# Performance work log

Measured on AMD Instinct MI355X. Metric: run time of the kernel, lower is better.

## Reference

```python
import jax, jax.numpy as jnp
import numpy as np


def _haar_filters():
    s = 1.0 / np.sqrt(2.0).astype(np.float32)
    l = jnp.array([s, s], dtype=jnp.float32)
    h = jnp.array([-s, s], dtype=jnp.float32)
    ll = jnp.outer(l, l)
    lh = jnp.outer(h, l)
    hl = jnp.outer(l, h)
    hh = jnp.outer(h, h)
    # module registers ll, -lh, -hl, hh as buffers
    return ll, -lh, -hl, hh


def setup_inputs() -> dict:
    key = jax.random.key(0)
    x = jax.random.normal(key, (16, 12, 512, 512), dtype=jnp.float32)
    fll, flh, fhl, fhh = _haar_filters()
    return {"x": x, "fll": fll, "flh": flh, "fhl": fhl, "fhh": fhh}


def _upfirdn_band(x, f):
    # upfirdn2d(band, f, up_factor=2, padding=(1,0,1,0)):
    #   2) zero pad: 1 on left of W, 1 on top of H
    #   3) valid conv with 2x2 FIR filter, applied per channel
    #   4) down_factor=1 interpolate -> identity
    B, C, H, W = x.shape
    up = jax.image.resize(x, (B, C, 2 * H, 2 * W), method="bilinear")
    p = jnp.pad(up, ((0, 0), (0, 0), (1, 0), (1, 0)))  # [B,C,2H+1,2W+1]
    w = jnp.tile(f[None, None].astype(x.dtype), (C, 1, 1, 1))  # depthwise [C,1,2,2]
    return jax.lax.conv_general_dilated(
        p, w, window_strides=(1, 1), padding="VALID",
        feature_group_count=C,
        dimension_numbers=("NCHW", "OIHW", "NCHW"),
    )  # [B,C,2H,2W]


def reference(x, fll, flh, fhl, fhh):
    ll, lh, hl, hh = jnp.split(x, 4, axis=1)  # input.chunk(4, 1)
    out = (_upfirdn_band(ll, fll)
           + _upfirdn_band(lh, flh)
           + _upfirdn_band(hl, fhl)
           + _upfirdn_band(hh, fhh))
    return out
```

## Files before the change

kernel.cpp:

```cpp
#include <hip/hip_runtime.h>

namespace {

constexpr int Hh = 512, Ww = 512, OH = 1024, OW = 1024;
constexpr int NB_Y = 256;
constexpr int NBC  = 48;
constexpr int NWG  = NB_Y * NBC;

typedef float f32x4 __attribute__((ext_vector_type(4)));

__global__ __launch_bounds__(256) void ihaar(
    const float* __restrict__ x,
    const float* __restrict__ f0,
    const float* __restrict__ f1,
    const float* __restrict__ f2,
    const float* __restrict__ f3,
    float* __restrict__ out)
{
  const int bid = blockIdx.x;
  const int wg  = (bid & 7) * (NWG / 8) + (bid >> 3);
  const int bc   = wg / NB_Y;
  const int yblk = wg - bc * NB_Y;
  const int b = bc / 3;
  const int c = bc - 3 * b;

  const int t    = threadIdx.x;
  const int lane = t & 63;
  const int wv   = t >> 6;
  const int half = wv & 1;
  const int ty   = wv >> 1;
  const int y    = 2 * yblk + ty;
  const int x0   = half * 256 + lane * 4;

  const float4 F[4] = { *(const float4*)f0, *(const float4*)f1,
                        *(const float4*)f2, *(const float4*)f3 };

  const int u0r = (y > 0) ? y - 1 : 0;
  const int u2r = (y < Hh - 1) ? y + 1 : y;
  const bool needL = (lane == 0)  && (half == 1);
  const bool needR = (lane == 63) && (half == 0);
  const bool le = (x0 == 0), re = (x0 == Ww - 4);
  const int sc = needL ? (x0 - 1) : (x0 + 4);

  float Pe0=0.f,Pe1=0.f,Pe2=0.f,Pe3=0.f, Po0=0.f,Po1=0.f,Po2=0.f,Po3=0.f;
  float Qe0=0.f,Qe1=0.f,Qe2=0.f,Qe3=0.f, Qo0=0.f,Qo1=0.f,Qo2=0.f,Qo3=0.f;
  float SPe=0.f,SPo=0.f,SQe=0.f,SQo=0.f;

#define BAND(g, Ae0,Ae1,Ae2,Ae3, Ao0,Ao1,Ao2,Ao3, Se, So) { \
    const float uu0 = F[g].x, uu1 = F[g].z; \
    float pa0, pa1, pb0, pb1, pb2; \
    if (y > 0) { pa0 = 0.75f*uu0 + 0.25f*uu1; pa1 = 0.25f*uu0 + 0.75f*uu1; } \
    else       { pa0 = 0.f;                   pa1 = uu1; } \
    if (y == 0)           { pb0 = 0.f;         pb1 = uu0 + 0.75f*uu1; pb2 = 0.25f*uu1; } \
    else if (y == Hh - 1) { pb0 = 0.25f*uu0;   pb1 = 0.75f*uu0 + uu1; pb2 = 0.f; } \
    else                  { pb0 = 0.25f*uu0;   pb1 = 0.75f*(uu0+uu1); pb2 = 0.25f*uu1; } \
    const float* Xp = x + (size_t)(b * 12 + (g) * 3 + c) * (Hh * Ww); \
    const f32x4 q0 = *(const f32x4*)(Xp + (size_t)u0r * Ww + x0); \
    const f32x4 q1 = *(const f32x4*)(Xp + (size_t)y   * Ww + x0); \
    const f32x4 q2 = *(const f32x4*)(Xp + (size_t)u2r * Ww + x0); \
    Ae0 += pa0*q0.x + pa1*q1.x;  Ae1 += pa0*q0.y + pa1*q1.y; \
    Ae2 += pa0*q0.z + pa1*q1.z;  Ae3 += pa0*q0.w + pa1*q1.w; \
    Ao0 += pb0*q0.x + pb1*q1.x + pb2*q2.x; \
    Ao1 += pb0*q0.y + pb1*q1.y + pb2*q2.y; \
    Ao2 += pb0*q0.z + pb1*q1.z + pb2*q2.z; \
    Ao3 += pb0*q0.w + pb1*q1.w + pb2*q2.w; \
    if (needL || needR) { \
      const float s0 = Xp[(size_t)u0r * Ww + sc]; \
      const float s1 = Xp[(size_t)y   * Ww + sc]; \
      const float s2 = Xp[(size_t)u2r * Ww + sc]; \
      Se += pa0*s0 + pa1*s1;  So += pb0*s0 + pb1*s1 + pb2*s2; \
    } \
  }

  BAND(0, Pe0,Pe1,Pe2,Pe3, Po0,Po1,Po2,Po3, SPe, SPo)
  BAND(1, Pe0,Pe1,Pe2,Pe3, Po0,Po1,Po2,Po3, SPe, SPo)
  BAND(2, Qe0,Qe1,Qe2,Qe3, Qo0,Qo1,Qo2,Qo3, SQe, SQo)
  BAND(3, Qe0,Qe1,Qe2,Qe3, Qo0,Qo1,Qo2,Qo3, SQe, SQo)
#undef BAND

  float PeL = __shfl_up(Pe3, 1),  PoL = __shfl_up(Po3, 1);
  float QeL = __shfl_up(Qe3, 1),  QoL = __shfl_up(Qo3, 1);
  float PeR = __shfl_down(Pe0, 1), PoR = __shfl_down(Po0, 1);
  float QeR = __shfl_down(Qe0, 1), QoR = __shfl_down(Qo0, 1);
  if (needL) { PeL = SPe; PoL = SPo; QeL = SQe; QoL = SQo; }
  if (needR) { PeR = SPe; PoR = SPo; QeR = SQe; QoR = SQo; }

  const float vp = F[0].y * __builtin_amdgcn_rcpf(F[0].x);
  const float vq = F[2].y * __builtin_amdgcn_rcpf(F[2].x);
  const float h0p = 0.75f + 0.25f*vp, h1p = 0.25f + 0.75f*vp;
  const float g0p = 0.25f, g1p = 0.75f*(1.f + vp), g2p = 0.25f*vp;
  const float h0q = 0.75f + 0.25f*vq, h1q = 0.25f + 0.75f*vq;
  const float g0q = 0.25f, g1q = 0.75f*(1.f + vq), g2q = 0.25f*vq;
  const float h0pa = le ? 0.f : h0p, h1pa = le ? vp : h1p;
  const float g0pa = le ? 0.f : g0p, g1pa = le ? (1.f + 0.75f*vp) : g1p;
  const float g1pd = re ? (0.75f + vp) : g1p, g2pd = re ? 0.f : g2p;
  const float h0qa = le ? 0.f : h0q, h1qa = le ? vq : h1q;
  const float g0qa = le ? 0.f : g0q, g1qa = le ? (1.f + 0.75f*vq) : g1q;
  const float g1qd = re ? (0.75f + vq) : g1q, g2qd = re ? 0.f : g2q;

  const float e0 = h0pa*PeL + h1pa*Pe0           + h0qa*QeL + h1qa*Qe0;
  const float e1 = g0pa*PeL + g1pa*Pe0 + g2p*Pe1 + g0qa*QeL + g1qa*Qe0 + g2q*Qe1;
  const float e2 = h0p*Pe0  + h1p*Pe1            + h0q*Qe0  + h1q*Qe1;
  const float e3 = g0p*Pe0  + g1p*Pe1  + g2p*Pe2 + g0q*Qe0  + g1q*Qe1  + g2q*Qe2;
  const float e4 = h0p*Pe1  + h1p*Pe2            + h0q*Qe1  + h1q*Qe2;
  const float e5 = g0p*Pe1  + g1p*Pe2  + g2p*Pe3 + g0q*Qe1  + g1q*Qe2  + g2q*Qe3;
  const float e6 = h0p*Pe2  + h1p*Pe3            + h0q*Qe2  + h1q*Qe3;
  const float e7 = g0p*Pe2  + g1pd*Pe3 + g2pd*PeR+ g0q*Qe2  + g1qd*Qe3 + g2qd*QeR;
  const float o0 = h0pa*PoL + h1pa*Po0           + h0qa*QoL + h1qa*Qo0;
  const float o1 = g0pa*PoL + g1pa*Po0 + g2p*Po1 + g0qa*QoL + g1qa*Qo0 + g2q*Qo1;
  const float o2 = h0p*Po0  + h1p*Po1            + h0q*Qo0  + h1q*Qo1;
  const float o3 = g0p*Po0  + g1p*Po1  + g2p*Po2 + g0q*Qo0  + g1q*Qo1  + g2q*Qo2;
  const float o4 = h0p*Po1  + h1p*Po2            + h0q*Qo1  + h1q*Qo2;
  const float o5 = g0p*Po1  + g1p*Po2  + g2p*Po3 + g0q*Qo1  + g1q*Qo2  + g2q*Qo3;
  const float o6 = h0p*Po2  + h1p*Po3            + h0q*Qo2  + h1q*Qo3;
  const float o7 = g0p*Po2  + g1pd*Po3 + g2pd*PoR+ g0q*Qo2  + g1qd*Qo3 + g2qd*QoR;

  float* op = out + ((size_t)bc * OH + 2 * y) * OW + 2 * x0;
  const f32x4 E0 = { e0, e1, e2, e3 };
  const f32x4 E1 = { e4, e5, e6, e7 };
  const f32x4 O0 = { o0, o1, o2, o3 };
  const f32x4 O1 = { o4, o5, o6, o7 };
  __builtin_nontemporal_store(E0, (f32x4*)op);
  __builtin_nontemporal_store(E1, (f32x4*)(op + 4));
  __builtin_nontemporal_store(O0, (f32x4*)(op + OW));
  __builtin_nontemporal_store(O1, (f32x4*)(op + OW + 4));
}

}

extern "C" void kernel_launch(void* const* d_in, const int* in_sizes, int n_in,
                              void* d_out, int out_size, void* d_ws, size_t ws_size,
                              hipStream_t stream) {
  const float* x   = (const float*)d_in[0];
  const float* fll = (const float*)d_in[1];
  const float* flh = (const float*)d_in[2];
  const float* fhl = (const float*)d_in[3];
  const float* fhh = (const float*)d_in[4];
  float* out = (float*)d_out;

  ihaar<<<dim3(NWG), 256, 0, stream>>>(x, fll, flh, fhl, fhh, out);
}
```

Measured before the change: 68.11 us.

## Process two input rows per thread to share vertical halo loads

```diff
diff --git a/kernel.cpp b/kernel.cpp
--- a/kernel.cpp
+++ b/kernel.cpp
@@ -3,9 +3,9 @@
 namespace {
 
 constexpr int Hh = 512, Ww = 512, OH = 1024, OW = 1024;
-constexpr int NB_Y = 256;
-constexpr int NBC  = 48;
-constexpr int NWG  = NB_Y * NBC;
+constexpr int NB_YP = 128;
+constexpr int NBC   = 48;
+constexpr int NWG   = NB_YP * NBC;
 
 typedef float f32x4 __attribute__((ext_vector_type(4)));
 
@@ -19,8 +19,8 @@
 {
   const int bid = blockIdx.x;
   const int wg  = (bid & 7) * (NWG / 8) + (bid >> 3);
-  const int bc   = wg / NB_Y;
-  const int yblk = wg - bc * NB_Y;
+  const int bc  = wg / NB_YP;
+  const int ybp = wg - bc * NB_YP;
   const int b = bc / 3;
   const int c = bc - 3 * b;
 
@@ -28,62 +28,97 @@
   const int lane = t & 63;
   const int wv   = t >> 6;
   const int half = wv & 1;
-  const int ty   = wv >> 1;
-  const int y    = 2 * yblk + ty;
+  const int sub  = wv >> 1;
+  const int y0   = 4 * ybp + 2 * sub;
+  const int y1   = y0 + 1;
   const int x0   = half * 256 + lane * 4;
+
+  const int rm = (y0 > 0) ? y0 - 1 : 0;
+  const int rt = (y1 < Hh - 1) ? y1 + 1 : Hh - 1;
+
+  const bool needL = (lane == 0)  && (half == 1);
+  const bool needR = (lane == 63) && (half == 0);
+  const bool seam  = needL || needR;
+  const bool le = (x0 == 0), re = (x0 == Ww - 4);
+  const int sc = needL ? (x0 - 1) : (x0 + 4);
+
+  const size_t HW = (size_t)Hh * Ww;
+  const float* Xa = x + (size_t)(b * 12 + c) * HW;
+  const float* Xb = Xa + 3 * HW;
+  const float* Xc = Xa + 6 * HW;
+  const float* Xd = Xa + 9 * HW;
+  const size_t om = (size_t)rm * Ww + x0;
+  const size_t orr = (size_t)y0 * Ww + x0;
+  const size_t os = (size_t)y1 * Ww + x0;
+  const size_t ot = (size_t)rt * Ww + x0;
+
+  const f32x4 qAm = *(const f32x4*)(Xa + om), qAr = *(const f32x4*)(Xa + orr);
+  const f32x4 qAs = *(const f32x4*)(Xa + os), qAt = *(const f32x4*)(Xa + ot);
+  const f32x4 qBm = *(const f32x4*)(Xb + om), qBr = *(const f32x4*)(Xb + orr);
+  const f32x4 qBs = *(const f32x4*)(Xb + os), qBt = *(const f32x4*)(Xb + ot);
+  const f32x4 qCm = *(const f32x4*)(Xc + om), qCr = *(const f32x4*)(Xc + orr);
+  const f32x4 qCs = *(const f32x4*)(Xc + os), qCt = *(const f32x4*)(Xc + ot);
+  const f32x4 qDm = *(const f32x4*)(Xd + om), qDr = *(const f32x4*)(Xd + orr);
+  const f32x4 qDs = *(const f32x4*)(Xd + os), qDt = *(const f32x4*)(Xd + ot);
+
+  float sAm=0.f,sAr=0.f,sAs=0.f,sAt=0.f, sBm=0.f,sBr=0.f,sBs=0.f,sBt=0.f;
+  float sCm=0.f,sCr=0.f,sCs=0.f,sCt=0.f, sDm=0.f,sDr=0.f,sDs=0.f,sDt=0.f;
+  if (seam) {
+    const size_t tm = (size_t)rm * Ww + sc, tr = (size_t)y0 * Ww + sc;
+    const size_t ts = (size_t)y1 * Ww + sc, tt = (size_t)rt * Ww + sc;
+    sAm = Xa[tm]; sAr = Xa[tr]; sAs = Xa[ts]; sAt = Xa[tt];
+    sBm = Xb[tm]; sBr = Xb[tr]; sBs = Xb[ts]; sBt = Xb[tt];
+    sCm = Xc[tm]; sCr = Xc[tr]; sCs = Xc[ts]; sCt = Xc[tt];
+    sDm = Xd[tm]; sDr = Xd[tr]; sDs = Xd[ts]; sDt = Xd[tt];
+  }
 
   const float4 F[4] = { *(const float4*)f0, *(const float4*)f1,
                         *(const float4*)f2, *(const float4*)f3 };
 
-  const int u0r = (y > 0) ? y - 1 : 0;
-  const int u2r = (y < Hh - 1) ? y + 1 : y;
-  const bool needL = (lane == 0)  && (half == 1);
-  const bool needR = (lane == 63) && (half == 0);
-  const bool le = (x0 == 0), re = (x0 == Ww - 4);
-  const int sc = needL ? (x0 - 1) : (x0 + 4);
+  float PE0a=0.f,PE0b=0.f,PE0c=0.f,PE0d=0.f, PO0a=0.f,PO0b=0.f,PO0c=0.f,PO0d=0.f;
+  float PE1a=0.f,PE1b=0.f,PE1c=0.f,PE1d=0.f, PO1a=0.f,PO1b=0.f,PO1c=0.f,PO1d=0.f;
+  float QE0a=0.f,QE0b=0.f,QE0c=0.f,QE0d=0.f, QO0a=0.f,QO0b=0.f,QO0c=0.f,QO0d=0.f;
+  float QE1a=0.f,QE1b=0.f,QE1c=0.f,QE1d=0.f, QO1a=0.f,QO1b=0.f,QO1c=0.f,QO1d=0.f;
+  float SPE0=0.f,SPO0=0.f,SPE1=0.f,SPO1=0.f;
+  float SQE0=0.f,SQO0=0.f,SQE1=0.f,SQO1=0.f;
 
-  float Pe0=0.f,Pe1=0.f,Pe2=0.f,Pe3=0.f, Po0=0.f,Po1=0.f,Po2=0.f,Po3=0.f;
-  float Qe0=0.f,Qe1=0.f,Qe2=0.f,Qe3=0.f, Qo0=0.f,Qo1=0.f,Qo2=0.f,Qo3=0.f;
-  float SPe=0.f,SPo=0.f,SQe=0.f,SQo=0.f;
-
-#define BAND(g, Ae0,Ae1,Ae2,Ae3, Ao0,Ao1,Ao2,Ao3, Se, So) { \
+#define BANDV(g, qm,qr,qs,qt, sm,sr,ss,st, GE0,GO0,GE1,GO1, SE0,SO0,SE1,SO1) { \
     const float uu0 = F[g].x, uu1 = F[g].z; \
-    float pa0, pa1, pb0, pb1, pb2; \
-    if (y > 0) { pa0 = 0.75f*uu0 + 0.25f*uu1; pa1 = 0.25f*uu0 + 0.75f*uu1; } \
-    else       { pa0 = 0.f;                   pa1 = uu1; } \
-    if (y == 0)           { pb0 = 0.f;         pb1 = uu0 + 0.75f*uu1; pb2 = 0.25f*uu1; } \
-    else if (y == Hh - 1) { pb0 = 0.25f*uu0;   pb1 = 0.75f*uu0 + uu1; pb2 = 0.f; } \
-    else                  { pb0 = 0.25f*uu0;   pb1 = 0.75f*(uu0+uu1); pb2 = 0.25f*uu1; } \
-    const float* Xp = x + (size_t)(b * 12 + (g) * 3 + c) * (Hh * Ww); \
-    const f32x4 q0 = *(const f32x4*)(Xp + (size_t)u0r * Ww + x0); \
-    const f32x4 q1 = *(const f32x4*)(Xp + (size_t)y   * Ww + x0); \
-    const f32x4 q2 = *(const f32x4*)(Xp + (size_t)u2r * Ww + x0); \
-    Ae0 += pa0*q0.x + pa1*q1.x;  Ae1 += pa0*q0.y + pa1*q1.y; \
-    Ae2 += pa0*q0.z + pa1*q1.z;  Ae3 += pa0*q0.w + pa1*q1.w; \
-    Ao0 += pb0*q0.x + pb1*q1.x + pb2*q2.x; \
-    Ao1 += pb0*q0.y + pb1*q1.y + pb2*q2.y; \
-    Ao2 += pb0*q0.z + pb1*q1.z + pb2*q2.z; \
-    Ao3 += pb0*q0.w + pb1*q1.w + pb2*q2.w; \
-    if (needL || needR) { \
-      const float s0 = Xp[(size_t)u0r * Ww + sc]; \
-      const float s1 = Xp[(size_t)y   * Ww + sc]; \
-      const float s2 = Xp[(size_t)u2r * Ww + sc]; \
-      Se += pa0*s0 + pa1*s1;  So += pb0*s0 + pb1*s1 + pb2*s2; \
+    const float pa0 = 0.75f*uu0 + 0.25f*uu1; \
+    const float pa1 = 0.25f*uu0 + 0.75f*uu1; \
+    const float eA0 = (y0 > 0) ? pa0 : 0.f; \
+    const float eA1 = (y0 > 0) ? pa1 : uu1; \
+    const float o00 = (y0 > 0) ? 0.25f*uu0 : 0.f; \
+    const float o01 = (y0 > 0) ? 0.75f*(uu0+uu1) : (uu0 + 0.75f*uu1); \
+    const float o02 = 0.25f*uu1; \
+    const float o10 = 0.25f*uu0; \
+    const float o11 = (y1 < Hh-1) ? 0.75f*(uu0+uu1) : (0.75f*uu0 + uu1); \
+    const float o12 = (y1 < Hh-1) ? 0.25f*uu1 : 0.f; \
+    GE0##a += eA0*qm.x + eA1*qr.x;  GE0##b += eA0*qm.y + eA1*qr.y; \
+    GE0##c += eA0*qm.z + eA1*qr.z;  GE0##d += eA0*qm.w + eA1*qr.w; \
+    GO0##a += o00*qm.x + o01*qr.x + o02*qs.x; \
+    GO0##b += o00*qm.y + o01*qr.y + o02*qs.y; \
+    GO0##c += o00*qm.z + o01*qr.z + o02*qs.z; \
+    GO0##d += o00*qm.w + o01*qr.w + o02*qs.w; \
+    GE1##a += pa0*qr.x + pa1*qs.x;  GE1##b += pa0*qr.y + pa1*qs.y; \
+    GE1##c += pa0*qr.z + pa1*qs.z;  GE1##d += pa0*qr.w + pa1*qs.w; \
+    GO1##a += o10*qr.x + o11*qs.x + o12*qt.x; \
+    GO1##b += o10*qr.y + o11*qs.y + o12*qt.y; \
+    GO1##c += o10*qr.z + o11*qs.z + o12*qt.z; \
+    GO1##d += o10*qr.w + o11*qs.w + o12*qt.w; \
+    if (seam) { \
+      SE0 += eA0*sm + eA1*sr; \
+      SO0 += o00*sm + o01*sr + o02*ss; \
+      SE1 += pa0*sr + pa1*ss; \
+      SO1 += o10*sr + o11*ss + o12*st; \
     } \
   }
 
-  BAND(0, Pe0,Pe1,Pe2,Pe3, Po0,Po1,Po2,Po3, SPe, SPo)
-  BAND(1, Pe0,Pe1,Pe2,Pe3, Po0,Po1,Po2,Po3, SPe, SPo)
-  BAND(2, Qe0,Qe1,Qe2,Qe3, Qo0,Qo1,Qo2,Qo3, SQe, SQo)
-  BAND(3, Qe0,Qe1,Qe2,Qe3, Qo0,Qo1,Qo2,Qo3, SQe, SQo)
-#undef BAND
-
-  float PeL = __shfl_up(Pe3, 1),  PoL = __shfl_up(Po3, 1);
-  float QeL = __shfl_up(Qe3, 1),  QoL = __shfl_up(Qo3, 1);
-  float PeR = __shfl_down(Pe0, 1), PoR = __shfl_down(Po0, 1);
-  float QeR = __shfl_down(Qe0, 1), QoR = __shfl_down(Qo0, 1);
-  if (needL) { PeL = SPe; PoL = SPo; QeL = SQe; QoL = SQo; }
-  if (needR) { PeR = SPe; PoR = SPo; QeR = SQe; QoR = SQo; }
+  BANDV(0, qAm,qAr,qAs,qAt, sAm,sAr,sAs,sAt, PE0,PO0,PE1,PO1, SPE0,SPO0,SPE1,SPO1)
+  BANDV(1, qBm,qBr,qBs,qBt, sBm,sBr,sBs,sBt, PE0,PO0,PE1,PO1, SPE0,SPO0,SPE1,SPO1)
+  BANDV(2, qCm,qCr,qCs,qCt, sCm,sCr,sCs,sCt, QE0,QO0,QE1,QO1, SQE0,SQO0,SQE1,SQO1)
+  BANDV(3, qDm,qDr,qDs,qDt, sDm,sDr,sDs,sDt, QE0,QO0,QE1,QO1, SQE0,SQO0,SQE1,SQO1)
+#undef BANDV
 
   const float vp = F[0].y * __builtin_amdgcn_rcpf(F[0].x);
   const float vq = F[2].y * __builtin_amdgcn_rcpf(F[2].x);
@@ -98,32 +133,32 @@
   const float g0qa = le ? 0.f : g0q, g1qa = le ? (1.f + 0.75f*vq) : g1q;
   const float g1qd = re ? (0.75f + vq) : g1q, g2qd = re ? 0.f : g2q;
 
-  const float e0 = h0pa*PeL + h1pa*Pe0           + h0qa*QeL + h1qa*Qe0;
-  const float e1 = g0pa*PeL + g1pa*Pe0 + g2p*Pe1 + g0qa*QeL + g1qa*Qe0 + g2q*Qe1;
-  const float e2 = h0p*Pe0  + h1p*Pe1            + h0q*Qe0  + h1q*Qe1;
-  const float e3 = g0p*Pe0  + g1p*Pe1  + g2p*Pe2 + g0q*Qe0  + g1q*Qe1  + g2q*Qe2;
-  const float e4 = h0p*Pe1  + h1p*Pe2            + h0q*Qe1  + h1q*Qe2;
-  const float e5 = g0p*Pe1  + g1p*Pe2  + g2p*Pe3 + g0q*Qe1  + g1q*Qe2  + g2q*Qe3;
-  const float e6 = h0p*Pe2  + h1p*Pe3            + h0q*Qe2  + h1q*Qe3;
-  const float e7 = g0p*Pe2  + g1pd*Pe3 + g2pd*PeR+ g0q*Qe2  + g1qd*Qe3 + g2qd*QeR;
-  const float o0 = h0pa*PoL + h1pa*Po0           + h0qa*QoL + h1qa*Qo0;
-  const float o1 = g0pa*PoL + g1pa*Po0 + g2p*Po1 + g0qa*QoL + g1qa*Qo0 + g2q*Qo1;
-  const float o2 = h0p*Po0  + h1p*Po1            + h0q*Qo0  + h1q*Qo1;
-  const float o3 = g0p*Po0  + g1p*Po1  + g2p*Po2 + g0q*Qo0  + g1q*Qo1  + g2q*Qo2;
-  const float o4 = h0p*Po1  + h1p*Po2            + h0q*Qo1  + h1q*Qo2;
-  const float o5 = g0p*Po1  + g1p*Po2  + g2p*Po3 + g0q*Qo1  + g1q*Qo2  + g2q*Qo3;
-  const float o6 = h0p*Po2  + h1p*Po3            + h0q*Qo2  + h1q*Qo3;
-  const float o7 = g0p*Po2  + g1pd*Po3 + g2pd*PoR+ g0q*Qo2  + g1qd*Qo3 + g2qd*QoR;
+  float* op = out + ((size_t)bc * OH + 2 * y0) * OW + 2 * x0;
 
-  float* op = out + ((size_t)bc * OH + 2 * y) * OW + 2 * x0;
-  const f32x4 E0 = { e0, e1, e2, e3 };
-  const f32x4 E1 = { e4, e5, e6, e7 };
-  const f32x4 O0 = { o0, o1, o2, o3 };
-  const f32x4 O1 = { o4, o5, o6, o7 };
-  __builtin_nontemporal_store(E0, (f32x4*)op);
-  __builtin_nontemporal_store(E1, (f32x4*)(op + 4));
-  __builtin_nontemporal_store(O0, (f32x4*)(op + OW));
-  __builtin_nontemporal_store(O1, (f32x4*)(op + OW + 4));
+#define HPASS(P0,P1,P2,P3, Q0,Q1,Q2,Q3, SP,SQ, rowp) { \
+    float PL = __shfl_up(P3, 1),  QL = __shfl_up(Q3, 1); \
+    float PR = __shfl_down(P0, 1), QR = __shfl_down(Q0, 1); \
+    if (needL) { PL = SP; QL = SQ; } \
+    if (needR) { PR = SP; QR = SQ; } \
+    const float z0 = h0pa*PL + h1pa*P0            + h0qa*QL + h1qa*Q0; \
+    const float z1 = g0pa*PL + g1pa*P0 + g2p*P1   + g0qa*QL + g1qa*Q0 + g2q*Q1; \
+    const float z2 = h0p*P0  + h1p*P1             + h0q*Q0  + h1q*Q1; \
+    const float z3 = g0p*P0  + g1p*P1  + g2p*P2   + g0q*Q0  + g1q*Q1  + g2q*Q2; \
+    const float z4 = h0p*P1  + h1p*P2             + h0q*Q1  + h1q*Q2; \
+    const float z5 = g0p*P1  + g1p*P2  + g2p*P3   + g0q*Q1  + g1q*Q2  + g2q*Q3; \
+    const float z6 = h0p*P2  + h1p*P3             + h0q*Q2  + h1q*Q3; \
+    const float z7 = g0p*P2  + g1pd*P3 + g2pd*PR  + g0q*Q2  + g1qd*Q3 + g2qd*QR; \
+    const f32x4 Z0 = { z0, z1, z2, z3 }; \
+    const f32x4 Z1 = { z4, z5, z6, z7 }; \
+    __builtin_nontemporal_store(Z0, (f32x4*)(rowp)); \
+    __builtin_nontemporal_store(Z1, (f32x4*)((rowp) + 4)); \
+  }
+
+  HPASS(PE0a,PE0b,PE0c,PE0d, QE0a,QE0b,QE0c,QE0d, SPE0,SQE0, op)
+  HPASS(PO0a,PO0b,PO0c,PO0d, QO0a,QO0b,QO0c,QO0d, SPO0,SQO0, op + OW)
+  HPASS(PE1a,PE1b,PE1c,PE1d, QE1a,QE1b,QE1c,QE1d, SPE1,SQE1, op + 2*OW)
+  HPASS(PO1a,PO1b,PO1c,PO1d, QO1a,QO1b,QO1c,QO1d, SPO1,SQO1, op + 3*OW)
+#undef HPASS
 }
 
 }
```

Result: slower. 87.27 us (+28.1%).
